# Kernel tuning notes

Hardware: AMD Instinct MI355X
Metric: run time of the kernel (lower is better)

The kernel has to match this reference:

```python
import jax, jax.numpy as jnp
import numpy as np

N, M, K, D = 8192, 64, 256, 16  # n_vecs, subvector_num, ksub (2**subvector_bits), dsub


def setup_inputs() -> dict:
    key = jax.random.key(0)
    k1, k2 = jax.random.split(key)
    vecs = jax.random.normal(k1, (N, M * D), dtype=jnp.float32)
    codebook = jax.random.normal(k2, (M, K, D), dtype=jnp.float32)
    return {"vecs": vecs, "codebook": codebook}


def reference(vecs, codebook):
    # quantization pipeline: code_selection -> get_index -> quantized_vecs
    n = vecs.shape[0]
    m, k, d = codebook.shape
    v = vecs.reshape(n, m, d)
    # proba = -||v - c||^2 computed via expansion (same math, no [N,M,K,D] broadcast)
    v2 = jnp.sum(v * v, axis=-1)[:, :, None]            # [N,M,1]
    c2 = jnp.sum(codebook * codebook, axis=-1)[None]    # [1,M,K]
    vc = jnp.einsum('nmd,mkd->nmk', v, codebook)        # [N,M,K]
    proba = -(v2 - 2.0 * vc + c2)
    # softmax is monotonic -> argmax(softmax(proba)) == argmax(proba)
    index = jnp.argmax(proba, axis=-1)                  # [N,M] int
    # quantized_vecs: one-hot scatter + matmul == gather of selected codewords
    quantized = codebook[jnp.arange(m)[None, :], index] # [N,M,D]
    return quantized.reshape(n, m * d)
```

## Files before the change

### kernel.cpp

```cpp
#include <hip/hip_runtime.h>
#include <math.h>

#define M_SUB 64
#define K_CODES 256
#define D_DIM 16
#define ROW_F 1024
#define THRGAP 0.0078125f
#define YS 8
#define MPB (M_SUB / YS)
#define NR 64

typedef __attribute__((ext_vector_type(8))) short short8;
typedef __attribute__((ext_vector_type(4))) float f32x4;

__device__ inline unsigned bfr(float x) {
    unsigned u = __builtin_bit_cast(unsigned, x);
    return (u + 0x7FFFu + ((u >> 16) & 1u)) >> 16;
}
__device__ inline float bff(unsigned h) { return __builtin_bit_cast(float, h << 16); }

template <int C> __device__ inline float dppf(float x) {
    return __builtin_bit_cast(float,
        __builtin_amdgcn_update_dpp(0, __builtin_bit_cast(int, x), C, 0xF, 0xF, true));
}
template <int C> __device__ inline int dppi(int x) {
    return __builtin_amdgcn_update_dpp(0, x, C, 0xF, 0xF, true);
}

__global__ __launch_bounds__(256, 4) void pq_mfma_kernel(
    const float* __restrict__ vecs, const float* __restrict__ cb,
    float* __restrict__ out, unsigned* __restrict__ meta, unsigned cap)
{
    const int m0  = blockIdx.y * MPB;
    const int nb  = blockIdx.x * NR;
    const int tid = threadIdx.x;
    const int w    = tid >> 6;
    const int lane = tid & 63;
    const int lr   = lane & 15;
    const int lg   = lane >> 4;

    __shared__ short BLDS[K_CODES * 40];
    __shared__ float NC2[K_CODES];

    unsigned* cnt  = meta;
    unsigned* list = meta + 1;

    const int rowA = nb + w * 16 + lr;
    const float* vbaseA = vecs + (size_t)rowA * ROW_F + (lg & 1) * 8;

    #pragma unroll 1
    for (int mi = 0; mi < MPB; ++mi) {
        const int m = m0 + mi;
        __syncthreads();
        {
            const float* cp = cb + ((size_t)m * K_CODES + tid) * D_DIM;
            float f[16];
            #pragma unroll
            for (int q = 0; q < 4; ++q) {
                float4 t4 = ((const float4*)cp)[q];
                f[q*4+0] = t4.x; f[q*4+1] = t4.y; f[q*4+2] = t4.z; f[q*4+3] = t4.w;
            }
            float c2 = 0.f;
            #pragma unroll
            for (int d = 0; d < 16; ++d) c2 = fmaf(f[d], f[d], c2);
            NC2[tid] = -c2;
            short hi[16], lo[16];
            #pragma unroll
            for (int d = 0; d < 16; ++d) {
                unsigned h = bfr(f[d]);
                hi[d] = (short)h;
                lo[d] = (short)bfr(f[d] - bff(h));
            }
            short* base = &BLDS[tid * 40];
            short8 v0 = { hi[0],hi[1],hi[2],hi[3],hi[4],hi[5],hi[6],hi[7] };
            short8 v1 = { hi[8],hi[9],hi[10],hi[11],hi[12],hi[13],hi[14],hi[15] };
            short8 v2 = { lo[0],lo[1],lo[2],lo[3],lo[4],lo[5],lo[6],lo[7] };
            short8 v3 = { lo[8],lo[9],lo[10],lo[11],lo[12],lo[13],lo[14],lo[15] };
            *(short8*)&base[0]  = v0; *(short8*)&base[8]  = v1;
            *(short8*)&base[16] = v2; *(short8*)&base[24] = v3;
        }
        __syncthreads();

        const float* vp = vbaseA + m * D_DIM;
        float f[8];
        {
            float4 a = ((const float4*)vp)[0], b4 = ((const float4*)vp)[1];
            f[0]=2.f*a.x; f[1]=2.f*a.y; f[2]=2.f*a.z; f[3]=2.f*a.w;
            f[4]=2.f*b4.x; f[5]=2.f*b4.y; f[6]=2.f*b4.z; f[7]=2.f*b4.w;
        }
        short hi[8], lo[8];
        #pragma unroll
        for (int e = 0; e < 8; ++e) {
            unsigned h = bfr(f[e]);
            hi[e] = (short)h;
            lo[e] = (short)bfr(f[e] - bff(h));
        }
        short8 H = { hi[0],hi[1],hi[2],hi[3],hi[4],hi[5],hi[6],hi[7] };
        short8 L = { lo[0],lo[1],lo[2],lo[3],lo[4],lo[5],lo[6],lo[7] };
        const bool hiSide = (lg < 2);
        short8 A1 = hiSide ? H : L;
        short8 A2 = hiSide ? L : H;

        f32x4 acc[16];
        #pragma unroll
        for (int kt = 0; kt < 16; ++kt) {
            short8 B = *(const short8*)&BLDS[(kt * 16 + lr) * 40 + lg * 8];
            float nv = NC2[kt * 16 + lr];
            f32x4 c0 = { nv, nv, nv, nv };
            c0 = __builtin_amdgcn_mfma_f32_16x16x32_bf16(A1, B, c0, 0, 0, 0);
            c0 = __builtin_amdgcn_mfma_f32_16x16x32_bf16(A2, B, c0, 0, 0, 0);
            acc[kt] = c0;
        }

        int kp0 = 0, kp1 = 0, kp2 = 0, kp3 = 0;
        #pragma unroll
        for (int p = 0; p < 4; ++p) {
            float b = acc[0][p];
            #pragma unroll
            for (int kt = 1; kt < 16; ++kt) b = fmaxf(b, acc[kt][p]);
            b = fmaxf(b, dppf<0xB1>(b));
            b = fmaxf(b, dppf<0x4E>(b));
            b = fmaxf(b, dppf<0x141>(b));
            b = fmaxf(b, dppf<0x140>(b));
            const float bthr = b - THRGAP;
            int c = 0, bk = 0x7FFFFFFF;
            #pragma unroll
            for (int kt = 15; kt >= 0; --kt) {
                bool cand = acc[kt][p] >= bthr;
                c += cand ? 1 : 0;
                bk = cand ? (kt * 16 + lr) : bk;
            }
            c += dppi<0xB1>(c);  bk = min(bk, dppi<0xB1>(bk));
            c += dppi<0x4E>(c);  bk = min(bk, dppi<0x4E>(bk));
            c += dppi<0x141>(c); bk = min(bk, dppi<0x141>(bk));
            c += dppi<0x140>(c); bk = min(bk, dppi<0x140>(bk));
            if (bk > 255) bk = 0;
            if (p == 0) kp0 = bk; else if (p == 1) kp1 = bk;
            else if (p == 2) kp2 = bk; else kp3 = bk;
            if (lr == 0 && c != 1) {
                unsigned idx = atomicAdd(cnt, 1u);
                if (idx < cap) list[idx] = ((unsigned)(nb + w * 16 + lg * 4 + p) << 6) | (unsigned)m;
            }
        }

        int psel = (lane >> 2) & 3;
        int t0 = (psel & 1) ? kp1 : kp0;
        int t1 = (psel & 1) ? kp3 : kp2;
        int kwin = (psel & 2) ? t1 : t0;
        const float4* src = (const float4*)(cb + ((size_t)m * K_CODES + kwin) * D_DIM);
        float4* dst = (float4*)(out + (size_t)(nb + w * 16 + (lane >> 2)) * ROW_F + m * D_DIM);
        dst[lane & 3] = src[lane & 3];
    }
}

__global__ __launch_bounds__(256) void pq_fixup_kernel(
    const float* __restrict__ vecs, const float* __restrict__ cb,
    float* __restrict__ out, const unsigned* __restrict__ meta, unsigned cap)
{
    unsigned cnt = meta[0];
    if (cnt > cap) cnt = cap;
    const unsigned nw  = (gridDim.x * blockDim.x) >> 6;
    const unsigned wid = (blockIdx.x * blockDim.x + threadIdx.x) >> 6;
    const int lane = threadIdx.x & 63;

    for (unsigned e = wid; e < cnt; e += nw) {
        unsigned ent = meta[1 + e];
        const int n = (int)(ent >> 6), m = (int)(ent & 63u);
        const float* vrow = vecs + (size_t)n * ROW_F + m * D_DIM;
        double vd[16];
        #pragma unroll
        for (int d = 0; d < 16; ++d) vd[d] = (double)vrow[d];
        double bs = -1e300; int bi = 0;
        #pragma unroll
        for (int j = 0; j < 4; ++j) {
            int k = lane * 4 + j;
            const float* cp = cb + ((size_t)m * K_CODES + k) * D_DIM;
            double vc = 0.0, c2 = 0.0;
            #pragma unroll
            for (int d = 0; d < 16; ++d) {
                double cd = (double)cp[d];
                vc = fma(vd[d], cd, vc);
                c2 = fma(cd, cd, c2);
            }
            double s = 2.0 * vc - c2;
            if (s > bs) { bs = s; bi = k; }
        }
        #pragma unroll
        for (int off = 32; off; off >>= 1) {
            double so = __shfl_xor(bs, off, 64);
            int    ko = __shfl_xor(bi, off, 64);
            if (so > bs || (so == bs && ko < bi)) { bs = so; bi = ko; }
        }
        if (lane < 4) {
            const float4* src = (const float4*)(cb + ((size_t)m * K_CODES + bi) * D_DIM);
            float4* dst = (float4*)(out + (size_t)n * ROW_F + m * D_DIM);
            dst[lane] = src[lane];
        }
    }
}

extern "C" void kernel_launch(void* const* d_in, const int* in_sizes, int n_in,
                              void* d_out, int out_size, void* d_ws, size_t ws_size,
                              hipStream_t stream) {
    const float* vecs = (const float*)d_in[0];
    const float* cb   = (const float*)d_in[1];
    float* out        = (float*)d_out;
    unsigned* meta    = (unsigned*)d_ws;
    unsigned cap      = (unsigned)(ws_size / 4) - 16;

    hipMemsetAsync(meta, 0, 4, stream);
    pq_mfma_kernel<<<dim3(8192 / NR, YS), 256, 0, stream>>>(vecs, cb, out, meta, cap);
    pq_fixup_kernel<<<256, 256, 0, stream>>>(vecs, cb, out, meta, cap);
}
```

Before: 66.91 us.

## Precompute packed codebook slices and double-buffer them into LDS via direct loads

A separate kernel converts the codebook once into bf16 hi/lo split slices with the negated norms, instead of every block redoing the conversion for each subvector. The main kernel now uses 512 threads and 128 rows per block. It stages the next slice into a second LDS buffer with global_load_lds while computing the current one, so only one barrier is needed per iteration. Selected indices are collected in LDS and the codeword gathers are written at the end as full 64-byte rows. The memset is replaced by a counter reset inside the convert kernel, and the fixup grid is shrunk. This adds an extra launch and workspace usage, and each block now needs more LDS.

```diff
diff --git a/kernel.cpp b/kernel.cpp
--- a/kernel.cpp
+++ b/kernel.cpp
@@ -8,7 +8,9 @@
 #define THRGAP 0.0078125f
 #define YS 8
 #define MPB (M_SUB / YS)
-#define NR 64
+#define NRB 128
+#define SLICE_B 21504
+#define BLDS_B 20480
 
 typedef __attribute__((ext_vector_type(8))) short short8;
 typedef __attribute__((ext_vector_type(4))) float f32x4;
@@ -27,67 +29,92 @@
     return __builtin_amdgcn_update_dpp(0, x, C, 0xF, 0xF, true);
 }
 
-__global__ __launch_bounds__(256, 4) void pq_mfma_kernel(
+__device__ inline void gl_lds16(const void* g, void* l) {
+    __builtin_amdgcn_global_load_lds((const __attribute__((address_space(1))) void*)g,
+                                     (__attribute__((address_space(3))) void*)l, 16, 0, 0);
+}
+__device__ inline void gl_lds4(const void* g, void* l) {
+    __builtin_amdgcn_global_load_lds((const __attribute__((address_space(1))) void*)g,
+                                     (__attribute__((address_space(3))) void*)l, 4, 0, 0);
+}
+
+__global__ __launch_bounds__(256) void pq_convert_kernel(
+    const float* __restrict__ cb, char* __restrict__ pk, unsigned* __restrict__ meta)
+{
+    const int m = blockIdx.x, k = threadIdx.x;
+    if (m == 0 && k == 0) meta[0] = 0;
+    const float* cp = cb + ((size_t)m * K_CODES + k) * D_DIM;
+    float f[16];
+    #pragma unroll
+    for (int q = 0; q < 4; ++q) {
+        float4 t4 = ((const float4*)cp)[q];
+        f[q*4+0] = t4.x; f[q*4+1] = t4.y; f[q*4+2] = t4.z; f[q*4+3] = t4.w;
+    }
+    float c2 = 0.f;
+    #pragma unroll
+    for (int d = 0; d < 16; ++d) c2 = fmaf(f[d], f[d], c2);
+    short hi[16], lo[16];
+    #pragma unroll
+    for (int d = 0; d < 16; ++d) {
+        unsigned h = bfr(f[d]);
+        hi[d] = (short)h;
+        lo[d] = (short)bfr(f[d] - bff(h));
+    }
+    char* base = pk + (size_t)m * SLICE_B + k * 80;
+    short8 v0 = { hi[0],hi[1],hi[2],hi[3],hi[4],hi[5],hi[6],hi[7] };
+    short8 v1 = { hi[8],hi[9],hi[10],hi[11],hi[12],hi[13],hi[14],hi[15] };
+    short8 v2 = { lo[0],lo[1],lo[2],lo[3],lo[4],lo[5],lo[6],lo[7] };
+    short8 v3 = { lo[8],lo[9],lo[10],lo[11],lo[12],lo[13],lo[14],lo[15] };
+    *(short8*)(base +  0) = v0; *(short8*)(base + 16) = v1;
+    *(short8*)(base + 32) = v2; *(short8*)(base + 48) = v3;
+    *(float*)(pk + (size_t)m * SLICE_B + BLDS_B + k * 4) = -c2;
+}
+
+__device__ inline void stage_slice(const char* g, char* lbuf, int tid, int w) {
+    gl_lds16(g + tid * 16,          lbuf + w * 1024);
+    gl_lds16(g + 8192 + tid * 16,   lbuf + 8192 + w * 1024);
+    if (tid < 256) {
+        gl_lds16(g + 16384 + tid * 16, lbuf + 16384 + w * 1024);
+        gl_lds4 (g + BLDS_B + tid * 4, lbuf + BLDS_B + w * 256);
+    }
+}
+
+__global__ __launch_bounds__(512, 4) void pq_mfma_kernel(
     const float* __restrict__ vecs, const float* __restrict__ cb,
-    float* __restrict__ out, unsigned* __restrict__ meta, unsigned cap)
+    float* __restrict__ out, const char* __restrict__ pk,
+    unsigned* __restrict__ meta, unsigned cap)
 {
     const int m0  = blockIdx.y * MPB;
-    const int nb  = blockIdx.x * NR;
+    const int nb  = blockIdx.x * NRB;
     const int tid = threadIdx.x;
     const int w    = tid >> 6;
     const int lane = tid & 63;
     const int lr   = lane & 15;
     const int lg   = lane >> 4;
 
-    __shared__ short BLDS[K_CODES * 40];
-    __shared__ float NC2[K_CODES];
+    __shared__ __align__(16) char BUF[2][SLICE_B];
+    __shared__ unsigned IDXs[MPB * 32];
 
     unsigned* cnt  = meta;
     unsigned* list = meta + 1;
 
-    const int rowA = nb + w * 16 + lr;
-    const float* vbaseA = vecs + (size_t)rowA * ROW_F + (lg & 1) * 8;
+    const float* vbaseA = vecs + (size_t)(nb + w * 16 + lr) * ROW_F + (lg & 1) * 8;
+    const char* pkm = pk + (size_t)m0 * SLICE_B;
+
+    stage_slice(pkm, BUF[0], tid, w);
+    __syncthreads();
 
     #pragma unroll 1
     for (int mi = 0; mi < MPB; ++mi) {
-        const int m = m0 + mi;
-        __syncthreads();
-        {
-            const float* cp = cb + ((size_t)m * K_CODES + tid) * D_DIM;
-            float f[16];
-            #pragma unroll
-            for (int q = 0; q < 4; ++q) {
-                float4 t4 = ((const float4*)cp)[q];
-                f[q*4+0] = t4.x; f[q*4+1] = t4.y; f[q*4+2] = t4.z; f[q*4+3] = t4.w;
-            }
-            float c2 = 0.f;
-            #pragma unroll
-            for (int d = 0; d < 16; ++d) c2 = fmaf(f[d], f[d], c2);
-            NC2[tid] = -c2;
-            short hi[16], lo[16];
-            #pragma unroll
-            for (int d = 0; d < 16; ++d) {
-                unsigned h = bfr(f[d]);
-                hi[d] = (short)h;
-                lo[d] = (short)bfr(f[d] - bff(h));
-            }
-            short* base = &BLDS[tid * 40];
-            short8 v0 = { hi[0],hi[1],hi[2],hi[3],hi[4],hi[5],hi[6],hi[7] };
-            short8 v1 = { hi[8],hi[9],hi[10],hi[11],hi[12],hi[13],hi[14],hi[15] };
-            short8 v2 = { lo[0],lo[1],lo[2],lo[3],lo[4],lo[5],lo[6],lo[7] };
-            short8 v3 = { lo[8],lo[9],lo[10],lo[11],lo[12],lo[13],lo[14],lo[15] };
-            *(short8*)&base[0]  = v0; *(short8*)&base[8]  = v1;
-            *(short8*)&base[16] = v2; *(short8*)&base[24] = v3;
-        }
-        __syncthreads();
-
-        const float* vp = vbaseA + m * D_DIM;
+        const int cur = mi & 1;
+        const float* vp = vbaseA + (size_t)(m0 + mi) * D_DIM;
+        float4 a4 = ((const float4*)vp)[0];
+        float4 b4 = ((const float4*)vp)[1];
+        if (mi + 1 < MPB) stage_slice(pkm + (size_t)(mi + 1) * SLICE_B, BUF[cur ^ 1], tid, w);
+
         float f[8];
-        {
-            float4 a = ((const float4*)vp)[0], b4 = ((const float4*)vp)[1];
-            f[0]=2.f*a.x; f[1]=2.f*a.y; f[2]=2.f*a.z; f[3]=2.f*a.w;
-            f[4]=2.f*b4.x; f[5]=2.f*b4.y; f[6]=2.f*b4.z; f[7]=2.f*b4.w;
-        }
+        f[0]=2.f*a4.x; f[1]=2.f*a4.y; f[2]=2.f*a4.z; f[3]=2.f*a4.w;
+        f[4]=2.f*b4.x; f[5]=2.f*b4.y; f[6]=2.f*b4.z; f[7]=2.f*b4.w;
         short hi[8], lo[8];
         #pragma unroll
         for (int e = 0; e < 8; ++e) {
@@ -101,55 +128,71 @@
         short8 A1 = hiSide ? H : L;
         short8 A2 = hiSide ? L : H;
 
+        const short* Bb = (const short*)BUF[cur];
+        const float* NC = (const float*)(BUF[cur] + BLDS_B);
+
         f32x4 acc[16];
         #pragma unroll
         for (int kt = 0; kt < 16; ++kt) {
-            short8 B = *(const short8*)&BLDS[(kt * 16 + lr) * 40 + lg * 8];
-            float nv = NC2[kt * 16 + lr];
+            short8 B = *(const short8*)&Bb[(kt * 16 + lr) * 40 + lg * 8];
+            float nv = NC[kt * 16 + lr];
             f32x4 c0 = { nv, nv, nv, nv };
             c0 = __builtin_amdgcn_mfma_f32_16x16x32_bf16(A1, B, c0, 0, 0, 0);
             c0 = __builtin_amdgcn_mfma_f32_16x16x32_bf16(A2, B, c0, 0, 0, 0);
             acc[kt] = c0;
         }
 
-        int kp0 = 0, kp1 = 0, kp2 = 0, kp3 = 0;
+        unsigned kp[4]; unsigned fl = 0;
         #pragma unroll
         for (int p = 0; p < 4; ++p) {
-            float b = acc[0][p];
-            #pragma unroll
-            for (int kt = 1; kt < 16; ++kt) b = fmaxf(b, acc[kt][p]);
+            float x0 = fmaxf(fmaxf(acc[0][p],  acc[1][p]),  acc[2][p]);
+            float x1 = fmaxf(fmaxf(acc[3][p],  acc[4][p]),  acc[5][p]);
+            float x2 = fmaxf(fmaxf(acc[6][p],  acc[7][p]),  acc[8][p]);
+            float x3 = fmaxf(fmaxf(acc[9][p],  acc[10][p]), acc[11][p]);
+            float x4 = fmaxf(fmaxf(acc[12][p], acc[13][p]), acc[14][p]);
+            float b  = fmaxf(fmaxf(fmaxf(x0, x1), x2), fmaxf(fmaxf(x3, x4), acc[15][p]));
             b = fmaxf(b, dppf<0xB1>(b));
             b = fmaxf(b, dppf<0x4E>(b));
             b = fmaxf(b, dppf<0x141>(b));
             b = fmaxf(b, dppf<0x140>(b));
             const float bthr = b - THRGAP;
-            int c = 0, bk = 0x7FFFFFFF;
+            unsigned Mm = 0;
             #pragma unroll
-            for (int kt = 15; kt >= 0; --kt) {
-                bool cand = acc[kt][p] >= bthr;
-                c += cand ? 1 : 0;
-                bk = cand ? (kt * 16 + lr) : bk;
+            for (int kt = 15; kt >= 0; --kt)
+                Mm = Mm + Mm + (acc[kt][p] >= bthr ? 1u : 0u);
+            int cl  = __popc(Mm);
+            int bkt = __ffs(Mm) - 1;
+            int bkv = Mm ? (bkt * 16 + lr) : 0x7FFFFFFF;
+            cl += dppi<0xB1>(cl);  bkv = min(bkv, dppi<0xB1>(bkv));
+            cl += dppi<0x4E>(cl);  bkv = min(bkv, dppi<0x4E>(bkv));
+            cl += dppi<0x141>(cl); bkv = min(bkv, dppi<0x141>(bkv));
+            cl += dppi<0x140>(cl); bkv = min(bkv, dppi<0x140>(bkv));
+            kp[p] = (unsigned)bkv & 255u;
+            fl |= (cl != 1) ? (1u << p) : 0u;
+        }
+        if (lr == 0) {
+            IDXs[mi * 32 + w * 4 + lg] = kp[0] | (kp[1] << 8) | (kp[2] << 16) | (kp[3] << 24);
+            if (fl) {
+                #pragma unroll
+                for (int p = 0; p < 4; ++p) if (fl & (1u << p)) {
+                    unsigned idx = atomicAdd(cnt, 1u);
+                    if (idx < cap)
+                        list[idx] = ((unsigned)(nb + w * 16 + lg * 4 + p) << 6) | (unsigned)(m0 + mi);
+                }
             }
-            c += dppi<0xB1>(c);  bk = min(bk, dppi<0xB1>(bk));
-            c += dppi<0x4E>(c);  bk = min(bk, dppi<0x4E>(bk));
-            c += dppi<0x141>(c); bk = min(bk, dppi<0x141>(bk));
-            c += dppi<0x140>(c); bk = min(bk, dppi<0x140>(bk));
-            if (bk > 255) bk = 0;
-            if (p == 0) kp0 = bk; else if (p == 1) kp1 = bk;
-            else if (p == 2) kp2 = bk; else kp3 = bk;
-            if (lr == 0 && c != 1) {
-                unsigned idx = atomicAdd(cnt, 1u);
-                if (idx < cap) list[idx] = ((unsigned)(nb + w * 16 + lg * 4 + p) << 6) | (unsigned)m;
-            }
-        }
-
-        int psel = (lane >> 2) & 3;
-        int t0 = (psel & 1) ? kp1 : kp0;
-        int t1 = (psel & 1) ? kp3 : kp2;
-        int kwin = (psel & 2) ? t1 : t0;
-        const float4* src = (const float4*)(cb + ((size_t)m * K_CODES + kwin) * D_DIM);
-        float4* dst = (float4*)(out + (size_t)(nb + w * 16 + (lane >> 2)) * ROW_F + m * D_DIM);
-        dst[lane & 3] = src[lane & 3];
+        }
+        __syncthreads();
+    }
+
+    const int row = tid >> 2, q = tid & 3;
+    #pragma unroll
+    for (int s = 0; s < 2; ++s) {
+        const int mi = q * 2 + s;
+        unsigned pk4 = IDXs[mi * 32 + (row >> 2)];
+        int k = (int)((pk4 >> ((row & 3) * 8)) & 255u);
+        const float4* src = (const float4*)(cb + ((size_t)(m0 + mi) * K_CODES + k) * D_DIM);
+        float4* dst = (float4*)(out + (size_t)(nb + row) * ROW_F + (size_t)(m0 + mi) * D_DIM);
+        dst[0] = src[0]; dst[1] = src[1]; dst[2] = src[2]; dst[3] = src[3];
     }
 }
 
@@ -205,10 +248,18 @@
     const float* vecs = (const float*)d_in[0];
     const float* cb   = (const float*)d_in[1];
     float* out        = (float*)d_out;
-    unsigned* meta    = (unsigned*)d_ws;
-    unsigned cap      = (unsigned)(ws_size / 4) - 16;
-
-    hipMemsetAsync(meta, 0, 4, stream);
-    pq_mfma_kernel<<<dim3(8192 / NR, YS), 256, 0, stream>>>(vecs, cb, out, meta, cap);
-    pq_fixup_kernel<<<256, 256, 0, stream>>>(vecs, cb, out, meta, cap);
-}
+    const int n_rows  = in_sizes[0] / ROW_F;
+
+    const size_t pk_bytes = (size_t)M_SUB * SLICE_B;
+    size_t pk_off = (ws_size > pk_bytes + 65536)
+                        ? ((ws_size - pk_bytes) & ~(size_t)255) : 0;
+    char* pk       = (char*)d_ws + pk_off;
+    unsigned* meta = (unsigned*)d_ws;
+    size_t cap_sz  = pk_off / 4;
+    unsigned cap   = cap_sz > 1048576 ? 1048576u
+                     : (cap_sz > 8 ? (unsigned)(cap_sz - 8) : 0u);
+
+    pq_convert_kernel<<<M_SUB, 256, 0, stream>>>(cb, pk, meta);
+    pq_mfma_kernel<<<dim3(n_rows / NRB, YS), 512, 0, stream>>>(vecs, cb, out, pk, meta, cap);
+    pq_fixup_kernel<<<64, 256, 0, stream>>>(vecs, cb, out, meta, cap);
+}
```

Measured after the change: 94.49 us. 1.41x slower.

## Precompute packed bf16 codebook and fuse fp64 fixup into MFMA kernel

Applied to the files above, without the earlier changes.

Adds a small kernel that converts the codebook once into hi/lo bf16 tiles laid out in MFMA operand order, with negated norms, in workspace. The main kernel then reads B operands straight from global memory with no LDS staging or block barriers. Each wave handles 32 rows for one subvector, and ambiguous rows are resolved in place with an fp64 rescan instead of an atomic list and a second kernel. This removes the memset, the atomics, the fixup launch and the repeated per-block codebook conversion. In exchange it relies on global/L2 loads for B, and warps with tied rows serialize inline.

```diff
diff --git a/kernel.cpp b/kernel.cpp
--- a/kernel.cpp
+++ b/kernel.cpp
@@ -6,9 +6,8 @@
 #define D_DIM 16
 #define ROW_F 1024
 #define THRGAP 0.0078125f
-#define YS 8
-#define MPB (M_SUB / YS)
-#define NR 64
+#define TILE_B 1088
+#define SLICE_B (16 * TILE_B)
 
 typedef __attribute__((ext_vector_type(8))) short short8;
 typedef __attribute__((ext_vector_type(4))) float f32x4;
@@ -27,67 +26,72 @@
     return __builtin_amdgcn_update_dpp(0, x, C, 0xF, 0xF, true);
 }
 
-__global__ __launch_bounds__(256, 4) void pq_mfma_kernel(
+__global__ __launch_bounds__(256) void pq_convert_kernel(
+    const float* __restrict__ cb, char* __restrict__ pk)
+{
+    const int m = blockIdx.x, k = threadIdx.x;
+    const float* cp = cb + ((size_t)m * K_CODES + k) * D_DIM;
+    float f[16];
+    #pragma unroll
+    for (int q = 0; q < 4; ++q) {
+        float4 t4 = ((const float4*)cp)[q];
+        f[q*4+0] = t4.x; f[q*4+1] = t4.y; f[q*4+2] = t4.z; f[q*4+3] = t4.w;
+    }
+    float c2 = 0.f;
+    #pragma unroll
+    for (int d = 0; d < 16; ++d) c2 = fmaf(f[d], f[d], c2);
+    short hi[16], lo[16];
+    #pragma unroll
+    for (int d = 0; d < 16; ++d) {
+        unsigned h = bfr(f[d]);
+        hi[d] = (short)h;
+        lo[d] = (short)bfr(f[d] - bff(h));
+    }
+    char* tb = pk + (size_t)m * SLICE_B + (k >> 4) * TILE_B;
+    const int lr = k & 15;
+    short8 v0 = { hi[0],hi[1],hi[2],hi[3],hi[4],hi[5],hi[6],hi[7] };
+    short8 v1 = { hi[8],hi[9],hi[10],hi[11],hi[12],hi[13],hi[14],hi[15] };
+    short8 v2 = { lo[0],lo[1],lo[2],lo[3],lo[4],lo[5],lo[6],lo[7] };
+    short8 v3 = { lo[8],lo[9],lo[10],lo[11],lo[12],lo[13],lo[14],lo[15] };
+    *(short8*)(tb +   0 + lr * 16) = v0;
+    *(short8*)(tb + 256 + lr * 16) = v1;
+    *(short8*)(tb + 512 + lr * 16) = v2;
+    *(short8*)(tb + 768 + lr * 16) = v3;
+    *(float*)(tb + 1024 + lr * 4) = -c2;
+}
+
+__global__ __launch_bounds__(256, 2) void pq_mfma_kernel(
     const float* __restrict__ vecs, const float* __restrict__ cb,
-    float* __restrict__ out, unsigned* __restrict__ meta, unsigned cap)
+    float* __restrict__ out, const char* __restrict__ pk)
 {
-    const int m0  = blockIdx.y * MPB;
-    const int nb  = blockIdx.x * NR;
-    const int tid = threadIdx.x;
+    const int tid  = threadIdx.x;
     const int w    = tid >> 6;
     const int lane = tid & 63;
     const int lr   = lane & 15;
     const int lg   = lane >> 4;
-
-    __shared__ short BLDS[K_CODES * 40];
-    __shared__ float NC2[K_CODES];
-
-    unsigned* cnt  = meta;
-    unsigned* list = meta + 1;
-
-    const int rowA = nb + w * 16 + lr;
-    const float* vbaseA = vecs + (size_t)rowA * ROW_F + (lg & 1) * 8;
-
-    #pragma unroll 1
-    for (int mi = 0; mi < MPB; ++mi) {
-        const int m = m0 + mi;
-        __syncthreads();
-        {
-            const float* cp = cb + ((size_t)m * K_CODES + tid) * D_DIM;
-            float f[16];
-            #pragma unroll
-            for (int q = 0; q < 4; ++q) {
-                float4 t4 = ((const float4*)cp)[q];
-                f[q*4+0] = t4.x; f[q*4+1] = t4.y; f[q*4+2] = t4.z; f[q*4+3] = t4.w;
-            }
-            float c2 = 0.f;
-            #pragma unroll
-            for (int d = 0; d < 16; ++d) c2 = fmaf(f[d], f[d], c2);
-            NC2[tid] = -c2;
-            short hi[16], lo[16];
-            #pragma unroll
-            for (int d = 0; d < 16; ++d) {
-                unsigned h = bfr(f[d]);
-                hi[d] = (short)h;
-                lo[d] = (short)bfr(f[d] - bff(h));
-            }
-            short* base = &BLDS[tid * 40];
-            short8 v0 = { hi[0],hi[1],hi[2],hi[3],hi[4],hi[5],hi[6],hi[7] };
-            short8 v1 = { hi[8],hi[9],hi[10],hi[11],hi[12],hi[13],hi[14],hi[15] };
-            short8 v2 = { lo[0],lo[1],lo[2],lo[3],lo[4],lo[5],lo[6],lo[7] };
-            short8 v3 = { lo[8],lo[9],lo[10],lo[11],lo[12],lo[13],lo[14],lo[15] };
-            *(short8*)&base[0]  = v0; *(short8*)&base[8]  = v1;
-            *(short8*)&base[16] = v2; *(short8*)&base[24] = v3;
-        }
-        __syncthreads();
-
-        const float* vp = vbaseA + m * D_DIM;
+    const int wid  = blockIdx.x * 4 + w;
+    const int m    = wid >> 8;
+    const int n0   = (wid & 255) * 32;
+
+    __shared__ unsigned IDXW[4][8];
+    __shared__ unsigned FLGW[4][8];
+
+    const char* pkm = pk + (size_t)m * SLICE_B;
+
+    float nc2v[16];
+    #pragma unroll
+    for (int kt = 0; kt < 16; ++kt)
+        nc2v[kt] = *(const float*)(pkm + kt * TILE_B + 1024 + lr * 4);
+
+    short8 A1[2], A2[2];
+    #pragma unroll
+    for (int t = 0; t < 2; ++t) {
+        const float* vp = vecs + (size_t)(n0 + t * 16 + lr) * ROW_F + m * D_DIM + (lg & 1) * 8;
+        float4 a4 = ((const float4*)vp)[0];
+        float4 b4 = ((const float4*)vp)[1];
         float f[8];
-        {
-            float4 a = ((const float4*)vp)[0], b4 = ((const float4*)vp)[1];
-            f[0]=2.f*a.x; f[1]=2.f*a.y; f[2]=2.f*a.z; f[3]=2.f*a.w;
-            f[4]=2.f*b4.x; f[5]=2.f*b4.y; f[6]=2.f*b4.z; f[7]=2.f*b4.w;
-        }
+        f[0]=2.f*a4.x; f[1]=2.f*a4.y; f[2]=2.f*a4.z; f[3]=2.f*a4.w;
+        f[4]=2.f*b4.x; f[5]=2.f*b4.y; f[6]=2.f*b4.z; f[7]=2.f*b4.w;
         short hi[8], lo[8];
         #pragma unroll
         for (int e = 0; e < 8; ++e) {
@@ -98,104 +102,109 @@
         short8 H = { hi[0],hi[1],hi[2],hi[3],hi[4],hi[5],hi[6],hi[7] };
         short8 L = { lo[0],lo[1],lo[2],lo[3],lo[4],lo[5],lo[6],lo[7] };
         const bool hiSide = (lg < 2);
-        short8 A1 = hiSide ? H : L;
-        short8 A2 = hiSide ? L : H;
-
-        f32x4 acc[16];
-        #pragma unroll
-        for (int kt = 0; kt < 16; ++kt) {
-            short8 B = *(const short8*)&BLDS[(kt * 16 + lr) * 40 + lg * 8];
-            float nv = NC2[kt * 16 + lr];
-            f32x4 c0 = { nv, nv, nv, nv };
-            c0 = __builtin_amdgcn_mfma_f32_16x16x32_bf16(A1, B, c0, 0, 0, 0);
-            c0 = __builtin_amdgcn_mfma_f32_16x16x32_bf16(A2, B, c0, 0, 0, 0);
-            acc[kt] = c0;
-        }
-
-        int kp0 = 0, kp1 = 0, kp2 = 0, kp3 = 0;
+        A1[t] = hiSide ? H : L;
+        A2[t] = hiSide ? L : H;
+    }
+
+    f32x4 acc[2][16];
+    #pragma unroll
+    for (int kt = 0; kt < 16; ++kt) {
+        short8 B = *(const short8*)(pkm + kt * TILE_B + lane * 16);
+        float nv = nc2v[kt];
+        f32x4 c0 = { nv, nv, nv, nv };
+        f32x4 c1 = { nv, nv, nv, nv };
+        c0 = __builtin_amdgcn_mfma_f32_16x16x32_bf16(A1[0], B, c0, 0, 0, 0);
+        c0 = __builtin_amdgcn_mfma_f32_16x16x32_bf16(A2[0], B, c0, 0, 0, 0);
+        c1 = __builtin_amdgcn_mfma_f32_16x16x32_bf16(A1[1], B, c1, 0, 0, 0);
+        c1 = __builtin_amdgcn_mfma_f32_16x16x32_bf16(A2[1], B, c1, 0, 0, 0);
+        acc[0][kt] = c0;
+        acc[1][kt] = c1;
+    }
+
+    #pragma unroll
+    for (int t = 0; t < 2; ++t) {
+        unsigned kp[4]; unsigned rf = 0;
         #pragma unroll
         for (int p = 0; p < 4; ++p) {
-            float b = acc[0][p];
-            #pragma unroll
-            for (int kt = 1; kt < 16; ++kt) b = fmaxf(b, acc[kt][p]);
+            float x0 = fmaxf(fmaxf(acc[t][0][p],  acc[t][1][p]),  acc[t][2][p]);
+            float x1 = fmaxf(fmaxf(acc[t][3][p],  acc[t][4][p]),  acc[t][5][p]);
+            float x2 = fmaxf(fmaxf(acc[t][6][p],  acc[t][7][p]),  acc[t][8][p]);
+            float x3 = fmaxf(fmaxf(acc[t][9][p],  acc[t][10][p]), acc[t][11][p]);
+            float x4 = fmaxf(fmaxf(acc[t][12][p], acc[t][13][p]), acc[t][14][p]);
+            float b  = fmaxf(fmaxf(fmaxf(x0, x1), x2), fmaxf(fmaxf(x3, x4), acc[t][15][p]));
             b = fmaxf(b, dppf<0xB1>(b));
             b = fmaxf(b, dppf<0x4E>(b));
             b = fmaxf(b, dppf<0x141>(b));
             b = fmaxf(b, dppf<0x140>(b));
             const float bthr = b - THRGAP;
-            int c = 0, bk = 0x7FFFFFFF;
+            unsigned Mm = 0;
             #pragma unroll
-            for (int kt = 15; kt >= 0; --kt) {
-                bool cand = acc[kt][p] >= bthr;
-                c += cand ? 1 : 0;
-                bk = cand ? (kt * 16 + lr) : bk;
+            for (int kt = 15; kt >= 0; --kt)
+                Mm = Mm + Mm + (acc[t][kt][p] >= bthr ? 1u : 0u);
+            int cl  = __popc(Mm);
+            int bkt = __ffs(Mm) - 1;
+            int bkv = Mm ? (bkt * 16 + lr) : 0x7FFFFFFF;
+            cl += dppi<0xB1>(cl);  bkv = min(bkv, dppi<0xB1>(bkv));
+            cl += dppi<0x4E>(cl);  bkv = min(bkv, dppi<0x4E>(bkv));
+            cl += dppi<0x141>(cl); bkv = min(bkv, dppi<0x141>(bkv));
+            cl += dppi<0x140>(cl); bkv = min(bkv, dppi<0x140>(bkv));
+            if (bkv > 255) bkv = 0;
+            kp[p] = (unsigned)bkv;
+            rf |= (cl != 1) ? (1u << p) : 0u;
+        }
+        if (lr == 0) {
+            IDXW[w][t * 4 + lg] = kp[0] | (kp[1] << 8) | (kp[2] << 16) | (kp[3] << 24);
+            FLGW[w][t * 4 + lg] = rf;
+        }
+    }
+
+    #pragma unroll 1
+    for (int e = 0; e < 8; ++e) {
+        unsigned rf = FLGW[w][e];
+        if (rf) {
+            #pragma unroll 1
+            for (int p = 0; p < 4; ++p) if (rf & (1u << p)) {
+                const int r = (e >> 2) * 16 + (e & 3) * 4 + p;
+                const int n = n0 + r;
+                const float* vrow = vecs + (size_t)n * ROW_F + m * D_DIM;
+                double vd[16];
+                #pragma unroll
+                for (int d = 0; d < 16; ++d) vd[d] = (double)vrow[d];
+                double bs = -1e300; int bi = 0;
+                #pragma unroll
+                for (int j = 0; j < 4; ++j) {
+                    int k = lane * 4 + j;
+                    const float* cp = cb + ((size_t)m * K_CODES + k) * D_DIM;
+                    double vc = 0.0, c2 = 0.0;
+                    #pragma unroll
+                    for (int d = 0; d < 16; ++d) {
+                        double cd = (double)cp[d];
+                        vc = fma(vd[d], cd, vc);
+                        c2 = fma(cd, cd, c2);
+                    }
+                    double s = 2.0 * vc - c2;
+                    if (s > bs) { bs = s; bi = k; }
+                }
+                #pragma unroll
+                for (int off = 32; off; off >>= 1) {
+                    double so = __shfl_xor(bs, off, 64);
+                    int    ko = __shfl_xor(bi, off, 64);
+                    if (so > bs || (so == bs && ko < bi)) { bs = so; bi = ko; }
+                }
+                if (lane == 0) ((char*)&IDXW[w][e])[p] = (char)bi;
             }
-            c += dppi<0xB1>(c);  bk = min(bk, dppi<0xB1>(bk));
-            c += dppi<0x4E>(c);  bk = min(bk, dppi<0x4E>(bk));
-            c += dppi<0x141>(c); bk = min(bk, dppi<0x141>(bk));
-            c += dppi<0x140>(c); bk = min(bk, dppi<0x140>(bk));
-            if (bk > 255) bk = 0;
-            if (p == 0) kp0 = bk; else if (p == 1) kp1 = bk;
-            else if (p == 2) kp2 = bk; else kp3 = bk;
-            if (lr == 0 && c != 1) {
-                unsigned idx = atomicAdd(cnt, 1u);
-                if (idx < cap) list[idx] = ((unsigned)(nb + w * 16 + lg * 4 + p) << 6) | (unsigned)m;
-            }
-        }
-
-        int psel = (lane >> 2) & 3;
-        int t0 = (psel & 1) ? kp1 : kp0;
-        int t1 = (psel & 1) ? kp3 : kp2;
-        int kwin = (psel & 2) ? t1 : t0;
-        const float4* src = (const float4*)(cb + ((size_t)m * K_CODES + kwin) * D_DIM);
-        float4* dst = (float4*)(out + (size_t)(nb + w * 16 + (lane >> 2)) * ROW_F + m * D_DIM);
-        dst[lane & 3] = src[lane & 3];
-    }
-}
-
-__global__ __launch_bounds__(256) void pq_fixup_kernel(
-    const float* __restrict__ vecs, const float* __restrict__ cb,
-    float* __restrict__ out, const unsigned* __restrict__ meta, unsigned cap)
-{
-    unsigned cnt = meta[0];
-    if (cnt > cap) cnt = cap;
-    const unsigned nw  = (gridDim.x * blockDim.x) >> 6;
-    const unsigned wid = (blockIdx.x * blockDim.x + threadIdx.x) >> 6;
-    const int lane = threadIdx.x & 63;
-
-    for (unsigned e = wid; e < cnt; e += nw) {
-        unsigned ent = meta[1 + e];
-        const int n = (int)(ent >> 6), m = (int)(ent & 63u);
-        const float* vrow = vecs + (size_t)n * ROW_F + m * D_DIM;
-        double vd[16];
-        #pragma unroll
-        for (int d = 0; d < 16; ++d) vd[d] = (double)vrow[d];
-        double bs = -1e300; int bi = 0;
-        #pragma unroll
-        for (int j = 0; j < 4; ++j) {
-            int k = lane * 4 + j;
-            const float* cp = cb + ((size_t)m * K_CODES + k) * D_DIM;
-            double vc = 0.0, c2 = 0.0;
-            #pragma unroll
-            for (int d = 0; d < 16; ++d) {
-                double cd = (double)cp[d];
-                vc = fma(vd[d], cd, vc);
-                c2 = fma(cd, cd, c2);
-            }
-            double s = 2.0 * vc - c2;
-            if (s > bs) { bs = s; bi = k; }
-        }
-        #pragma unroll
-        for (int off = 32; off; off >>= 1) {
-            double so = __shfl_xor(bs, off, 64);
-            int    ko = __shfl_xor(bi, off, 64);
-            if (so > bs || (so == bs && ko < bi)) { bs = so; bi = ko; }
-        }
-        if (lane < 4) {
-            const float4* src = (const float4*)(cb + ((size_t)m * K_CODES + bi) * D_DIM);
-            float4* dst = (float4*)(out + (size_t)n * ROW_F + m * D_DIM);
-            dst[lane] = src[lane];
-        }
+        }
+    }
+
+    #pragma unroll
+    for (int s = 0; s < 2; ++s) {
+        const int r = s * 16 + (lane >> 2);
+        unsigned e4 = IDXW[w][r >> 2];
+        const int k = (int)((e4 >> ((r & 3) * 8)) & 255u);
+        const float4* src = (const float4*)(cb + ((size_t)m * K_CODES + k) * D_DIM);
+        float4 val = src[lane & 3];
+        float4* dst = (float4*)(out + (size_t)(n0 + r) * ROW_F + m * D_DIM);
+        dst[lane & 3] = val;
     }
 }
 
@@ -205,10 +214,8 @@
     const float* vecs = (const float*)d_in[0];
     const float* cb   = (const float*)d_in[1];
     float* out        = (float*)d_out;
-    unsigned* meta    = (unsigned*)d_ws;
-    unsigned cap      = (unsigned)(ws_size / 4) - 16;
-
-    hipMemsetAsync(meta, 0, 4, stream);
-    pq_mfma_kernel<<<dim3(8192 / NR, YS), 256, 0, stream>>>(vecs, cb, out, meta, cap);
-    pq_fixup_kernel<<<256, 256, 0, stream>>>(vecs, cb, out, meta, cap);
-}
+    char* pk          = (char*)d_ws;
+
+    pq_convert_kernel<<<M_SUB, 256, 0, stream>>>(cb, pk);
+    pq_mfma_kernel<<<4096, 256, 0, stream>>>(vecs, cb, out, pk);
+}
```

Result: faster. 60.09 us (-10.2%).
